# Kernel optimization log

Measured on AMD Instinct MI355X. Metric: run time of the kernel, lower is better.

Reference implementation:

```python
import jax, jax.numpy as jnp
import numpy as np

N, E, G = 20000, 320000, 64
F, ED, H, HID, DL, DOUT = 128, 32, 300, 600, 256, 128
BN_INV = np.float32(1.0 / np.sqrt(1.0 + 1e-5))  # eval-mode BatchNorm, running stats (0,1)
EPS = 1e-7


def setup_inputs() -> dict:
    key = jax.random.key(0)
    ks = jax.random.split(key, 24)
    rn = lambda k, shape, s=0.05: (jax.random.normal(k, shape, jnp.float32) * s)
    inp = {
        "x": rn(ks[0], (N, F), 1.0),
        "edge_attr": rn(ks[1], (E, ED), 1.0),
        "edge_index": jax.random.randint(ks[2], (2, E), 0, N),
        "batch": jnp.sort(jax.random.randint(ks[3], (N,), 0, G)),
        # GENConv params (lin_src/lin_edge/lin_dst have bias=False in PyG)
        "W_src": rn(ks[4], (F, H)),
        "W_edge": rn(ks[5], (ED, H)),
        "W_dst": rn(ks[6], (F, H)),
        # GENConv internal MLP: [H, 2H, 2H, H], Linear -> ReLU -> BatchNorm between
        "W1": rn(ks[7], (H, HID)), "b1": jnp.zeros((HID,), jnp.float32),
        "g1": jnp.ones((HID,), jnp.float32), "be1": jnp.zeros((HID,), jnp.float32),
        "W2": rn(ks[8], (HID, HID)), "b2": jnp.zeros((HID,), jnp.float32),
        "g2": jnp.ones((HID,), jnp.float32), "be2": jnp.zeros((HID,), jnp.float32),
        "W3": rn(ks[9], (HID, H)), "b3": jnp.zeros((H,), jnp.float32),
        # encoder head: Linear(H,256) -> ReLU -> Linear(256, d_out)
        "L1": rn(ks[10], (H, DL)), "bl1": jnp.zeros((DL,), jnp.float32),
        "L2": rn(ks[11], (DL, DOUT)), "bl2": jnp.zeros((DOUT,), jnp.float32),
    }
    return inp


def reference(x, edge_attr, W_src, W_edge, W_dst, W1, b1, g1, be1, W2, b2, g2, be2,
              W3, b3, L1, bl1, L2, bl2, edge_index, batch):
    src, dst = edge_index[0], edge_index[1]
    h = x @ W_src                                   # [N,H]
    e = edge_attr @ W_edge                          # [E,H]
    msg = jax.nn.relu(h[src] + e) + EPS             # [E,H]
    # softmax aggregation over incoming edges, per destination node, per channel (t=1)
    m = jax.ops.segment_max(msg, dst, num_segments=N)          # [N,H]
    ex = jnp.exp(msg - m[dst])                                 # [E,H]
    denom = jax.ops.segment_sum(ex, dst, num_segments=N)       # [N,H]
    alpha = ex / denom[dst]
    agg = jax.ops.segment_sum(msg * alpha, dst, num_segments=N)  # [N,H]
    out = agg + x @ W_dst                                        # residual with lin_dst(x)
    # GENConv MLP (act_first: Linear -> ReLU -> BN), eval-mode BN
    h1 = jax.nn.relu(out @ W1 + b1) * BN_INV * g1 + be1
    h2 = jax.nn.relu(h1 @ W2 + b2) * BN_INV * g2 + be2
    out = h2 @ W3 + b3                                           # [N,H]
    # encoder linear stack (dropout = identity in eval)
    out = jax.nn.relu(out @ L1 + bl1)
    out = out @ L2 + bl2                                         # [N, d_out]
    # global mean pool over graphs
    cnt = jax.ops.segment_sum(jnp.ones((N,), jnp.float32), batch, num_segments=G)
    pooled = jax.ops.segment_sum(out, batch, num_segments=G) / jnp.maximum(cnt, 1.0)[:, None]
    return pooled
```

## Files before the change

kernel.cpp:

```cpp
#include <hip/hip_runtime.h>
#include <stdint.h>
#include <stddef.h>

#define N_NODES  20000
#define N_EDGES  320000
#define N_GRAPH  64
#define F_IN     128
#define E_DIM    32
#define H_DIM    300
#define HID_DIM  600
#define DL_DIM   256
#define DOUT_DIM 128
#define BN_INV_F 0.9999950000374997f
#define EPS_MSG  1e-7f

typedef _Float16 f16;
typedef __attribute__((ext_vector_type(8))) _Float16 f16x8;
typedef __attribute__((ext_vector_type(4))) _Float16 f16x4;
typedef __attribute__((ext_vector_type(4))) float f32x4;

#define GLOAD_LDS16(gp, lp) \
    __builtin_amdgcn_global_load_lds( \
        (const __attribute__((address_space(1))) void*)(gp), \
        (__attribute__((address_space(3))) void*)(lp), 16, 0, 0)

template<bool HAS_BIAS, bool RELU, bool BN, int OUT_MODE, bool DUAL_A>
__global__ __launch_bounds__(256)
void hgemm(const f16* __restrict__ A, const f16* __restrict__ A2,
           const f16* __restrict__ Bt,
           const float* __restrict__ bias, const float* __restrict__ gamma,
           const float* __restrict__ beta,
           void* __restrict__ O1, void* __restrict__ O2,
           int M, int Nreal, int Kpad, int ostride, int npad)
{
    __shared__ __align__(16) f16 As[64][32];
    __shared__ __align__(16) f16 Bs[64][32];
    const int tid  = threadIdx.x;
    const int bm   = blockIdx.y * 64;
    const int bn   = blockIdx.x * 64;
    const int wave = tid >> 6;
    const int lane = tid & 63;
    const int wm   = (wave >> 1) * 32;
    const int wn   = (wave & 1) * 32;
    const int fr   = lane & 15;
    const int kg   = lane >> 4;
    const int srow = tid >> 2;
    const int cg   = tid & 3;
    const int gsw  = (cg - (srow >> 1)) & 3;

    const f32x4 z = {0.f, 0.f, 0.f, 0.f};
    f32x4 acc[2][2] = {{z, z}, {z, z}};

    const f16* Asrc  = A + (size_t)(bm + srow) * Kpad + gsw * 8;
    const f16* Bsrc  = Bt + (size_t)(bn + srow) * Kpad + gsw * 8;
    const f16* A2src = DUAL_A ? (A2 + (size_t)(bm + srow) * Kpad + gsw * 8) : nullptr;
    f16* AsDst = &As[0][0] + (size_t)tid * 8;
    f16* BsDst = &Bs[0][0] + (size_t)tid * 8;
    const bool avalid = (bm + srow) < M;
    const f16x8 zf = {(f16)0, (f16)0, (f16)0, (f16)0,
                      (f16)0, (f16)0, (f16)0, (f16)0};

    const int ra0 = wm + fr,      ra1 = wm + 16 + fr;
    const int rb0 = wn + fr,      rb1 = wn + 16 + fr;
    const f16* a0p = &As[ra0][(((ra0 >> 1) + kg) & 3) * 8];
    const f16* a1p = &As[ra1][(((ra1 >> 1) + kg) & 3) * 8];
    const f16* b0p = &Bs[rb0][(((rb0 >> 1) + kg) & 3) * 8];
    const f16* b1p = &Bs[rb1][(((rb1 >> 1) + kg) & 3) * 8];

    for (int k0 = 0; k0 < Kpad; k0 += 32) {
        if (DUAL_A) {
            f16x8 va = zf;
            if (avalid)
                va = *(const f16x8*)Asrc + *(const f16x8*)A2src;
            *(f16x8*)AsDst = va;
            GLOAD_LDS16(Bsrc, BsDst);
            if (DUAL_A) { Asrc += 32; A2src += 32; }
        } else {
            GLOAD_LDS16(Asrc, AsDst);
            GLOAD_LDS16(Bsrc, BsDst);
            Asrc += 32;
        }
        Bsrc += 32;
        __syncthreads();
        f16x8 a0 = *(const f16x8*)a0p;
        f16x8 a1 = *(const f16x8*)a1p;
        f16x8 b0 = *(const f16x8*)b0p;
        f16x8 b1 = *(const f16x8*)b1p;
        acc[0][0] = __builtin_amdgcn_mfma_f32_16x16x32_f16(a0, b0, acc[0][0], 0, 0, 0);
        acc[0][1] = __builtin_amdgcn_mfma_f32_16x16x32_f16(a0, b1, acc[0][1], 0, 0, 0);
        acc[1][0] = __builtin_amdgcn_mfma_f32_16x16x32_f16(a1, b0, acc[1][0], 0, 0, 0);
        acc[1][1] = __builtin_amdgcn_mfma_f32_16x16x32_f16(a1, b1, acc[1][1], 0, 0, 0);
        __syncthreads();
    }

    #pragma unroll
    for (int mi = 0; mi < 2; ++mi) {
        #pragma unroll
        for (int r = 0; r < 4; ++r) {
            int row = bm + wm + mi * 16 + kg * 4 + r;
            if (row >= M) continue;
            #pragma unroll
            for (int ni = 0; ni < 2; ++ni) {
                int col = bn + wn + ni * 16 + fr;
                float v = acc[mi][ni][r];
                if (OUT_MODE == 2) {
                    if (col < 300)
                        ((f16*)O1)[(size_t)row * 304 + col] = (f16)v;
                    else if (col < 600)
                        ((f16*)O2)[(size_t)row * 320 + (col - 300)] = (f16)v;
                    else if (col < 620)
                        ((f16*)O2)[(size_t)row * 320 + (col - 300)] = (f16)0.f;
                } else {
                    if (col < Nreal) {
                        if (HAS_BIAS) v += bias[col];
                        if (RELU)     v = fmaxf(v, 0.f);
                        if (BN)       v = v * (BN_INV_F * gamma[col]) + beta[col];
                        if (OUT_MODE == 0)
                            ((float*)O1)[(size_t)row * ostride + col] = v;
                        else
                            ((f16*)O1)[(size_t)row * ostride + col] = (f16)v;
                    } else if (OUT_MODE == 1 && col < npad) {
                        ((f16*)O1)[(size_t)row * ostride + col] = (f16)0.f;
                    }
                }
            }
        }
    }
}

#define XB_N   640000
#define WSD_N  76800
#define WT1_N  192000
#define WT2_N  364800
#define WT3_N  182400
#define WL1_N  81920
#define WL2_N  32768
#define WET_N  9728
#define ZC_N   20000
#define ZP_N   8256
#define CAST_TOTAL (XB_N+WSD_N+WT1_N+WT2_N+WT3_N+WL1_N+WL2_N+WET_N+ZC_N+ZP_N)

__global__ __launch_bounds__(256)
void cast_all(const float* __restrict__ x,
              const float* __restrict__ Wsrc, const float* __restrict__ Wdst,
              const float* __restrict__ W1, const float* __restrict__ W2,
              const float* __restrict__ W3, const float* __restrict__ L1,
              const float* __restrict__ L2, const float* __restrict__ We,
              f16* __restrict__ xb,
              f16* __restrict__ Wt_sd, f16* __restrict__ Wt1,
              f16* __restrict__ Wt2, f16* __restrict__ Wt3,
              f16* __restrict__ WtL1, f16* __restrict__ WtL2,
              f16* __restrict__ Wet,
              int* __restrict__ cnts, float* __restrict__ pool,
              float* __restrict__ cnt)
{
    int t = blockIdx.x * 256 + threadIdx.x;
    if (t < XB_N) {
        float4 v = ((const float4*)x)[t];
        f16x4 o = {(f16)v.x, (f16)v.y, (f16)v.z, (f16)v.w};
        ((f16x4*)xb)[t] = o;
        return;
    }
    t -= XB_N;
    if (t < WSD_N) {
        int n = t / 128, k = t % 128;
        const float* W = (n < 300) ? Wsrc : Wdst;
        int nn = (n < 300) ? n : n - 300;
        Wt_sd[t] = (f16)W[(size_t)k * 300 + nn];
        return;
    }
    t -= WSD_N;
    if (t < WT1_N) {
        int n = t / 320, k = t % 320;
        Wt1[t] = (f16)((k < 300) ? W1[(size_t)k * 600 + n] : 0.f);
        return;
    }
    t -= WT1_N;
    if (t < WT2_N) {
        int n = t / 608, k = t % 608;
        Wt2[t] = (f16)((k < 600) ? W2[(size_t)k * 600 + n] : 0.f);
        return;
    }
    t -= WT2_N;
    if (t < WT3_N) {
        int n = t / 608, k = t % 608;
        Wt3[t] = (f16)((k < 600) ? W3[(size_t)k * 300 + n] : 0.f);
        return;
    }
    t -= WT3_N;
    if (t < WL1_N) {
        int n = t / 320, k = t % 320;
        WtL1[t] = (f16)((k < 300) ? L1[(size_t)k * 256 + n] : 0.f);
        return;
    }
    t -= WL1_N;
    if (t < WL2_N) {
        int n = t / 256, k = t % 256;
        WtL2[t] = (f16)L2[(size_t)k * 128 + n];
        return;
    }
    t -= WL2_N;
    if (t < WET_N) {
        int n = t / 32, k = t % 32;
        Wet[t] = (f16)((n < 300) ? We[(size_t)k * 300 + n] : 0.f);
        return;
    }
    t -= WET_N;
    if (t < ZC_N) { cnts[t] = 0; return; }
    t -= ZC_N;
    if (t < ZP_N) {
        if (t < 8192) pool[t] = 0.f;
        else          cnt[t - 8192] = 0.f;
    }
}

__global__ __launch_bounds__(256)
void hist_kernel(const int* __restrict__ ei, int* __restrict__ counts)
{
    for (int e = blockIdx.x * 256 + threadIdx.x; e < N_EDGES; e += gridDim.x * 256)
        atomicAdd(&counts[ei[N_EDGES + e]], 1);
}

__global__ __launch_bounds__(256)
void scan1_kernel(const int* __restrict__ counts, int* __restrict__ rowptr,
                  int* __restrict__ bsum)
{
    __shared__ int sd[256];
    int tid = threadIdx.x;
    int i = blockIdx.x * 256 + tid;
    int v = (i < N_NODES) ? counts[i] : 0;
    sd[tid] = v;
    __syncthreads();
    #pragma unroll
    for (int off = 1; off < 256; off <<= 1) {
        int t = (tid >= off) ? sd[tid - off] : 0;
        __syncthreads();
        sd[tid] += t;
        __syncthreads();
    }
    if (i < N_NODES) rowptr[i + 1] = sd[tid];
    if (tid == 255) bsum[blockIdx.x] = sd[255];
}

__global__ __launch_bounds__(128)
void scan2_kernel(const int* __restrict__ bsum, int* __restrict__ boffs, int nb)
{
    __shared__ int sd[128];
    int tid = threadIdx.x;
    int v = (tid < nb) ? bsum[tid] : 0;
    sd[tid] = v;
    __syncthreads();
    #pragma unroll
    for (int off = 1; off < 128; off <<= 1) {
        int t = (tid >= off) ? sd[tid - off] : 0;
        __syncthreads();
        sd[tid] += t;
        __syncthreads();
    }
    if (tid < nb) boffs[tid] = sd[tid] - v;
}

__global__ __launch_bounds__(256)
void scan3_kernel(int* __restrict__ rowptr, int* __restrict__ shadow,
                  const int* __restrict__ boffs)
{
    int i = blockIdx.x * 256 + threadIdx.x;
    if (i < N_NODES) {
        int v = rowptr[i + 1] + boffs[blockIdx.x];
        rowptr[i + 1] = v;
        shadow[i + 1] = v;
    }
    if (i == 0) { rowptr[0] = 0; shadow[0] = 0; }
}

__global__ __launch_bounds__(256)
void scatter_gather(const float* __restrict__ ea, const int* __restrict__ ei,
                    int* __restrict__ shadow, f16* __restrict__ eaf,
                    int* __restrict__ srcs)
{
    int e = blockIdx.x * 256 + threadIdx.x;
    if (e >= N_EDGES) return;
    int d = ei[N_EDGES + e];
    int pos = atomicAdd(&shadow[d], 1);
    srcs[pos] = ei[e];
    const float4* src = (const float4*)(ea + (size_t)e * E_DIM);
    f16* dst = eaf + (size_t)pos * E_DIM;
    #pragma unroll
    for (int q = 0; q < 8; ++q) {
        float4 v = src[q];
        f16x4 o = {(f16)v.x, (f16)v.y, (f16)v.z, (f16)v.w};
        ((f16x4*)dst)[q] = o;
    }
}

#define NPB 10
#define CHK 32
#define ELDS_STRIDE 308

__global__ __launch_bounds__(320, 1)
void agg_mfma(const f16* __restrict__ hf, const f16* __restrict__ eaf,
              const int* __restrict__ srcs, const int* __restrict__ rptr,
              const f16* __restrict__ Wet, f16* __restrict__ aggb)
{
    __shared__ __align__(16) f16 As[CHK][40];
    __shared__ __align__(16) f16 e_lds[CHK * ELDS_STRIDE];
    __shared__ int s_lds[CHK];

    const int tid  = threadIdx.x;
    const int w    = tid >> 6;
    const int lane = tid & 63;
    const int fr   = lane & 15;
    const int kg   = lane >> 4;
    const int c    = tid;
    const bool act = c < H_DIM;
    const int cc   = c < 304 ? c : 303;

    const int n0 = blockIdx.x * NPB;
    const int n1 = n0 + NPB;
    const int P0 = rptr[n0];
    const int P1 = rptr[n1];

    f16x8 bf0, bf1, bf2, bf3;
    {
        int t0 = w;
        bf0 = *(const f16x8*)(Wet + (size_t)(t0 * 16 + fr) * 32 + kg * 8);
        bf1 = *(const f16x8*)(Wet + (size_t)((t0 + 5) * 16 + fr) * 32 + kg * 8);
        bf2 = *(const f16x8*)(Wet + (size_t)((t0 + 10) * 16 + fr) * 32 + kg * 8);
        if (t0 + 15 < 19)
            bf3 = *(const f16x8*)(Wet + (size_t)((t0 + 15) * 16 + fr) * 32 + kg * 8);
    }

    const f32x4 z4 = {0.f, 0.f, 0.f, 0.f};

    int n_cur = n0;
    int e_end = (n_cur < n1) ? rptr[n_cur + 1] : 0x7fffffff;
    float num = 0.f, den = 0.f;

    auto flush = [&]() {
        float agg = den > 0.f ? num / den : 0.f;
        aggb[(size_t)n_cur * 320 + c] = act ? (f16)agg : (f16)0.f;
        num = 0.f; den = 0.f;
        ++n_cur;
        e_end = (n_cur < n1) ? rptr[n_cur + 1] : 0x7fffffff;
    };

    for (int ck = P0; ck < P1; ck += CHK) {
        const int cend = min(ck + CHK, P1);
        if (tid < 128) {
            int row = tid >> 2;
            int kq  = (tid & 3) * 8;
            int p   = ck + row;
            if (p >= N_EDGES) p = N_EDGES - 1;
            *(f16x8*)&As[row][kq] = *(const f16x8*)(eaf + (size_t)p * E_DIM + kq);
        } else if (tid < 128 + CHK) {
            int j = tid - 128;
            int p = ck + j;
            s_lds[j] = srcs[p < N_EDGES ? p : N_EDGES - 1];
        }
        __syncthreads();
        {
            f16x8 af0 = *(const f16x8*)&As[fr][kg * 8];
            f16x8 af1 = *(const f16x8*)&As[16 + fr][kg * 8];
            #pragma unroll
            for (int i = 0; i < 4; ++i) {
                int t = w + 5 * i;
                if (t >= 19) continue;
                f16x8 bf = (i == 0) ? bf0 : (i == 1) ? bf1 : (i == 2) ? bf2 : bf3;
                #pragma unroll
                for (int mi = 0; mi < 2; ++mi) {
                    f16x8 af = (mi == 0) ? af0 : af1;
                    f32x4 d = __builtin_amdgcn_mfma_f32_16x16x32_f16(af, bf, z4, 0, 0, 0);
                    int col = t * 16 + fr;
                    int rbase = mi * 16 + kg * 4;
                    #pragma unroll
                    for (int r = 0; r < 4; ++r)
                        e_lds[(size_t)(rbase + r) * ELDS_STRIDE + col] = (f16)d[r];
                }
            }
        }
        __syncthreads();
        for (int ck2 = ck; ck2 < cend; ck2 += 16) {
            float hv[16], ev[16];
            #pragma unroll
            for (int j = 0; j < 16; ++j) {
                int idx = (ck2 - ck) + j;
                int s = s_lds[idx];
                hv[j] = (float)hf[(size_t)s * 304 + cc];
                ev[j] = (float)e_lds[(size_t)idx * ELDS_STRIDE + cc];
            }
            #pragma unroll
            for (int j = 0; j < 16; ++j) {
                int p = ck2 + j;
                if (p < cend) {
                    while (p == e_end) flush();
                    float msg = fmaxf(hv[j] + ev[j], 0.f) + EPS_MSG;
                    float ex = __expf(msg);
                    den += ex;
                    num += msg * ex;
                }
            }
        }
        __syncthreads();
    }
    while (n_cur < n1) flush();
}

#define POOL_NPB 128
__global__ __launch_bounds__(128)
void pool_seg(const float* __restrict__ out3, const int* __restrict__ batch,
              float* __restrict__ pooled, float* __restrict__ cnt)
{
    int c = threadIdx.x;
    int n0 = blockIdx.x * POOL_NPB;
    int n1 = min(n0 + POOL_NPB, N_NODES);
    int g = batch[n0];
    float s = 0.f, cn = 0.f;
    for (int n = n0; n < n1; ++n) {
        int gn = batch[n];
        if (gn != g) {
            atomicAdd(&pooled[(size_t)g * DOUT_DIM + c], s);
            if (c == 0) atomicAdd(&cnt[g], cn);
            g = gn; s = 0.f; cn = 0.f;
        }
        s += out3[(size_t)n * DOUT_DIM + c];
        cn += 1.f;
    }
    atomicAdd(&pooled[(size_t)g * DOUT_DIM + c], s);
    if (c == 0) atomicAdd(&cnt[g], cn);
}

__global__ __launch_bounds__(256)
void finalize_kernel(const float* __restrict__ pooled, const float* __restrict__ cnt,
                     float* __restrict__ out)
{
    int i = blockIdx.x * 256 + threadIdx.x;
    if (i >= N_GRAPH * DOUT_DIM) return;
    out[i] = pooled[i] / fmaxf(cnt[i / DOUT_DIM], 1.f);
}

extern "C" void kernel_launch(void* const* d_in, const int* in_sizes, int n_in,
                              void* d_out, int out_size, void* d_ws, size_t ws_size,
                              hipStream_t stream)
{
    const float* x      = (const float*)d_in[0];
    const float* ea     = (const float*)d_in[1];
    const int*   eidx   = (const int*)d_in[2];
    const int*   batch  = (const int*)d_in[3];
    const float* W_src  = (const float*)d_in[4];
    const float* W_edge = (const float*)d_in[5];
    const float* W_dst  = (const float*)d_in[6];
    const float* W1     = (const float*)d_in[7];
    const float* b1     = (const float*)d_in[8];
    const float* g1     = (const float*)d_in[9];
    const float* be1    = (const float*)d_in[10];
    const float* W2     = (const float*)d_in[11];
    const float* b2     = (const float*)d_in[12];
    const float* g2     = (const float*)d_in[13];
    const float* be2    = (const float*)d_in[14];
    const float* W3     = (const float*)d_in[15];
    const float* b3     = (const float*)d_in[16];
    const float* L1     = (const float*)d_in[17];
    const float* bl1    = (const float*)d_in[18];
    const float* L2     = (const float*)d_in[19];
    const float* bl2    = (const float*)d_in[20];
    float* out = (float*)d_out;
    char* ws = (char*)d_ws;

    f16*   ws_h     = (f16*)  (ws + 0);
    f16*   ws_b2b   = (f16*)  (ws + 0);
    float* ws_out3  = (float*)(ws + 0);
    f16*   ws_eaf   = (f16*)  (ws + 24320000);
    f16*   ws_b1b   = (f16*)  (ws + 24320000);
    f16*   ws_out1b = (f16*)  (ws + 24320000);
    f16*   ws_out2b = (f16*)  (ws + 37120000);
    f16*   ws_aggb  = (f16*)  (ws + 44800000);
    f16*   ws_out0b = (f16*)  (ws + 65280000);
    f16*   ws_xb    = (f16*)  (ws + 78080000);
    f16*   ws_wtsd  = (f16*)  (ws + 83200000);
    f16*   ws_wt1   = (f16*)  (ws + 83353600);
    f16*   ws_wt2   = (f16*)  (ws + 83737600);
    f16*   ws_wt3   = (f16*)  (ws + 84467200);
    f16*   ws_wtl1  = (f16*)  (ws + 84832000);
    f16*   ws_wtl2  = (f16*)  (ws + 84995840);
    f16*   ws_wet   = (f16*)  (ws + 85061376);
    int*   ws_cnts  = (int*)  (ws + 85080832);
    int*   ws_rptr  = (int*)  (ws + 85240832);
    int*   ws_shad  = (int*)  (ws + 85320848);
    int*   ws_srcs  = (int*)  (ws + 86600848);
    float* ws_pool  = (float*)(ws + 87880848);
    float* ws_cnt   = (float*)(ws + 87913616);
    int*   ws_bsum  = (int*)  (ws + 87913872);
    int*   ws_boffs = (int*)  (ws + 87914384);

    dim3 blk(256);

    cast_all<<<(CAST_TOTAL + 255) / 256, blk, 0, stream>>>(
        x, W_src, W_dst, W1, W2, W3, L1, L2, W_edge,
        ws_xb, ws_wtsd, ws_wt1, ws_wt2, ws_wt3, ws_wtl1, ws_wtl2, ws_wet,
        ws_cnts, ws_pool, ws_cnt);

    hgemm<false, false, false, 2, false><<<dim3(10, 313), blk, 0, stream>>>(
        ws_xb, nullptr, ws_wtsd, nullptr, nullptr, nullptr, ws_h, ws_out0b,
        N_NODES, 600, 128, 304, 608);

    hist_kernel<<<512, blk, 0, stream>>>(eidx, ws_cnts);
    {
        int nb = (N_NODES + 255) / 256;
        scan1_kernel<<<nb, blk, 0, stream>>>(ws_cnts, ws_rptr, ws_bsum);
        scan2_kernel<<<1, dim3(128), 0, stream>>>(ws_bsum, ws_boffs, nb);
        scan3_kernel<<<nb, blk, 0, stream>>>(ws_rptr, ws_shad, ws_boffs);
    }
    scatter_gather<<<(N_EDGES + 255) / 256, blk, 0, stream>>>(
        ea, eidx, ws_shad, ws_eaf, ws_srcs);

    agg_mfma<<<N_NODES / NPB, dim3(320), 0, stream>>>(
        ws_h, ws_eaf, ws_srcs, ws_rptr, ws_wet, ws_aggb);

    hgemm<true, true, true, 1, true><<<dim3(10, 313), blk, 0, stream>>>(
        ws_aggb, ws_out0b, ws_wt1, b1, g1, be1, ws_b1b, nullptr,
        N_NODES, 600, 320, 608, 608);
    hgemm<true, true, true, 1, false><<<dim3(10, 313), blk, 0, stream>>>(
        ws_b1b, nullptr, ws_wt2, b2, g2, be2, ws_b2b, nullptr,
        N_NODES, 600, 608, 608, 608);
    hgemm<true, false, false, 1, false><<<dim3(5, 313), blk, 0, stream>>>(
        ws_b2b, nullptr, ws_wt3, b3, nullptr, nullptr, ws_out1b, nullptr,
        N_NODES, 300, 608, 320, 320);
    hgemm<true, true, false, 1, false><<<dim3(4, 313), blk, 0, stream>>>(
        ws_out1b, nullptr, ws_wtl1, bl1, nullptr, nullptr, ws_out2b, nullptr,
        N_NODES, 256, 320, 256, 256);
    hgemm<true, false, false, 0, false><<<dim3(2, 313), blk, 0, stream>>>(
        ws_out2b, nullptr, ws_wtl2, bl2, nullptr, nullptr, ws_out3, nullptr,
        N_NODES, 128, 256, 128, 128);

    pool_seg<<<(N_NODES + POOL_NPB - 1) / POOL_NPB, dim3(128), 0, stream>>>(
        ws_out3, batch, ws_pool, ws_cnt);
    finalize_kernel<<<(N_GRAPH * DOUT_DIM + 255) / 256, blk, 0, stream>>>(
        ws_pool, ws_cnt, out);
}
```

Before: 338.6 us.

## Fuse residual into aggregation, fuse pooling into last GEMM, merge scan passes

The aggregation kernel now adds its softmax result directly into the lin_dst residual buffer, so the first MLP GEMM loads a single A operand through global_load_lds instead of summing two buffers in registers. The final linear GEMM scatters its outputs with atomicAdd into per-graph pool sums, which removes the fp32 out3 buffer and the pool_seg kernel. Graph counts are recomputed in finalize by binary search on the sorted batch array. The three-pass scan becomes two passes, with each block serially summing the preceding block sums. The trade-off is heavy atomic contention on the 64x128 pool array (20000 rows onto 64 graphs).

```diff
diff --git a/kernel.cpp b/kernel.cpp
--- a/kernel.cpp
+++ b/kernel.cpp
@@ -24,13 +24,13 @@
         (const __attribute__((address_space(1))) void*)(gp), \
         (__attribute__((address_space(3))) void*)(lp), 16, 0, 0)
 
-template<bool HAS_BIAS, bool RELU, bool BN, int OUT_MODE, bool DUAL_A>
-__global__ __launch_bounds__(256)
-void hgemm(const f16* __restrict__ A, const f16* __restrict__ A2,
-           const f16* __restrict__ Bt,
+template<bool HAS_BIAS, bool RELU, bool BN, int OUT_MODE>
+__global__ __launch_bounds__(256)
+void hgemm(const f16* __restrict__ A, const f16* __restrict__ Bt,
            const float* __restrict__ bias, const float* __restrict__ gamma,
            const float* __restrict__ beta,
            void* __restrict__ O1, void* __restrict__ O2,
+           const int* __restrict__ batchp,
            int M, int Nreal, int Kpad, int ostride, int npad)
 {
     __shared__ __align__(16) f16 As[64][32];
@@ -51,14 +51,10 @@
     const f32x4 z = {0.f, 0.f, 0.f, 0.f};
     f32x4 acc[2][2] = {{z, z}, {z, z}};
 
-    const f16* Asrc  = A + (size_t)(bm + srow) * Kpad + gsw * 8;
-    const f16* Bsrc  = Bt + (size_t)(bn + srow) * Kpad + gsw * 8;
-    const f16* A2src = DUAL_A ? (A2 + (size_t)(bm + srow) * Kpad + gsw * 8) : nullptr;
+    const f16* Asrc = A + (size_t)(bm + srow) * Kpad + gsw * 8;
+    const f16* Bsrc = Bt + (size_t)(bn + srow) * Kpad + gsw * 8;
     f16* AsDst = &As[0][0] + (size_t)tid * 8;
     f16* BsDst = &Bs[0][0] + (size_t)tid * 8;
-    const bool avalid = (bm + srow) < M;
-    const f16x8 zf = {(f16)0, (f16)0, (f16)0, (f16)0,
-                      (f16)0, (f16)0, (f16)0, (f16)0};
 
     const int ra0 = wm + fr,      ra1 = wm + 16 + fr;
     const int rb0 = wn + fr,      rb1 = wn + 16 + fr;
@@ -68,18 +64,9 @@
     const f16* b1p = &Bs[rb1][(((rb1 >> 1) + kg) & 3) * 8];
 
     for (int k0 = 0; k0 < Kpad; k0 += 32) {
-        if (DUAL_A) {
-            f16x8 va = zf;
-            if (avalid)
-                va = *(const f16x8*)Asrc + *(const f16x8*)A2src;
-            *(f16x8*)AsDst = va;
-            GLOAD_LDS16(Bsrc, BsDst);
-            if (DUAL_A) { Asrc += 32; A2src += 32; }
-        } else {
-            GLOAD_LDS16(Asrc, AsDst);
-            GLOAD_LDS16(Bsrc, BsDst);
-            Asrc += 32;
-        }
+        GLOAD_LDS16(Asrc, AsDst);
+        GLOAD_LDS16(Bsrc, BsDst);
+        Asrc += 32;
         Bsrc += 32;
         __syncthreads();
         f16x8 a0 = *(const f16x8*)a0p;
@@ -110,6 +97,11 @@
                         ((f16*)O2)[(size_t)row * 320 + (col - 300)] = (f16)v;
                     else if (col < 620)
                         ((f16*)O2)[(size_t)row * 320 + (col - 300)] = (f16)0.f;
+                } else if (OUT_MODE == 3) {
+                    if (col < Nreal) {
+                        if (HAS_BIAS) v += bias[col];
+                        atomicAdd(&((float*)O2)[(size_t)batchp[row] * DOUT_DIM + col], v);
+                    }
                 } else {
                     if (col < Nreal) {
                         if (HAS_BIAS) v += bias[col];
@@ -137,7 +129,7 @@
 #define WL2_N  32768
 #define WET_N  9728
 #define ZC_N   20000
-#define ZP_N   8256
+#define ZP_N   8192
 #define CAST_TOTAL (XB_N+WSD_N+WT1_N+WT2_N+WT3_N+WL1_N+WL2_N+WET_N+ZC_N+ZP_N)
 
 __global__ __launch_bounds__(256)
@@ -151,8 +143,7 @@
               f16* __restrict__ Wt2, f16* __restrict__ Wt3,
               f16* __restrict__ WtL1, f16* __restrict__ WtL2,
               f16* __restrict__ Wet,
-              int* __restrict__ cnts, float* __restrict__ pool,
-              float* __restrict__ cnt)
+              int* __restrict__ cnts, float* __restrict__ pooled)
 {
     int t = blockIdx.x * 256 + threadIdx.x;
     if (t < XB_N) {
@@ -208,10 +199,7 @@
     t -= WET_N;
     if (t < ZC_N) { cnts[t] = 0; return; }
     t -= ZC_N;
-    if (t < ZP_N) {
-        if (t < 8192) pool[t] = 0.f;
-        else          cnt[t - 8192] = 0.f;
-    }
+    if (t < ZP_N) pooled[t] = 0.f;
 }
 
 __global__ __launch_bounds__(256)
@@ -222,8 +210,8 @@
 }
 
 __global__ __launch_bounds__(256)
-void scan1_kernel(const int* __restrict__ counts, int* __restrict__ rowptr,
-                  int* __restrict__ bsum)
+void scan_a(const int* __restrict__ counts, int* __restrict__ rowptr,
+            int* __restrict__ bsum)
 {
     __shared__ int sd[256];
     int tid = threadIdx.x;
@@ -242,31 +230,21 @@
     if (tid == 255) bsum[blockIdx.x] = sd[255];
 }
 
-__global__ __launch_bounds__(128)
-void scan2_kernel(const int* __restrict__ bsum, int* __restrict__ boffs, int nb)
-{
-    __shared__ int sd[128];
+__global__ __launch_bounds__(256)
+void scan_b(int* __restrict__ rowptr, int* __restrict__ shadow,
+            const int* __restrict__ bsum)
+{
+    __shared__ int off_s;
     int tid = threadIdx.x;
-    int v = (tid < nb) ? bsum[tid] : 0;
-    sd[tid] = v;
+    if (tid == 0) {
+        int o = 0;
+        for (int b = 0; b < (int)blockIdx.x; ++b) o += bsum[b];
+        off_s = o;
+    }
     __syncthreads();
-    #pragma unroll
-    for (int off = 1; off < 128; off <<= 1) {
-        int t = (tid >= off) ? sd[tid - off] : 0;
-        __syncthreads();
-        sd[tid] += t;
-        __syncthreads();
-    }
-    if (tid < nb) boffs[tid] = sd[tid] - v;
-}
-
-__global__ __launch_bounds__(256)
-void scan3_kernel(int* __restrict__ rowptr, int* __restrict__ shadow,
-                  const int* __restrict__ boffs)
-{
-    int i = blockIdx.x * 256 + threadIdx.x;
+    int i = blockIdx.x * 256 + tid;
     if (i < N_NODES) {
-        int v = rowptr[i + 1] + boffs[blockIdx.x];
+        int v = rowptr[i + 1] + off_s;
         rowptr[i + 1] = v;
         shadow[i + 1] = v;
     }
@@ -300,7 +278,7 @@
 __global__ __launch_bounds__(320, 1)
 void agg_mfma(const f16* __restrict__ hf, const f16* __restrict__ eaf,
               const int* __restrict__ srcs, const int* __restrict__ rptr,
-              const f16* __restrict__ Wet, f16* __restrict__ aggb)
+              const f16* __restrict__ Wet, f16* __restrict__ out0b)
 {
     __shared__ __align__(16) f16 As[CHK][40];
     __shared__ __align__(16) f16 e_lds[CHK * ELDS_STRIDE];
@@ -338,7 +316,10 @@
 
     auto flush = [&]() {
         float agg = den > 0.f ? num / den : 0.f;
-        aggb[(size_t)n_cur * 320 + c] = act ? (f16)agg : (f16)0.f;
+        if (act) {
+            size_t idx = (size_t)n_cur * 320 + c;
+            out0b[idx] = (f16)(agg + (float)out0b[idx]);
+        }
         num = 0.f; den = 0.f;
         ++n_cur;
         e_end = (n_cur < n1) ? rptr[n_cur + 1] : 0x7fffffff;
@@ -405,37 +386,25 @@
     while (n_cur < n1) flush();
 }
 
-#define POOL_NPB 128
-__global__ __launch_bounds__(128)
-void pool_seg(const float* __restrict__ out3, const int* __restrict__ batch,
-              float* __restrict__ pooled, float* __restrict__ cnt)
-{
-    int c = threadIdx.x;
-    int n0 = blockIdx.x * POOL_NPB;
-    int n1 = min(n0 + POOL_NPB, N_NODES);
-    int g = batch[n0];
-    float s = 0.f, cn = 0.f;
-    for (int n = n0; n < n1; ++n) {
-        int gn = batch[n];
-        if (gn != g) {
-            atomicAdd(&pooled[(size_t)g * DOUT_DIM + c], s);
-            if (c == 0) atomicAdd(&cnt[g], cn);
-            g = gn; s = 0.f; cn = 0.f;
-        }
-        s += out3[(size_t)n * DOUT_DIM + c];
-        cn += 1.f;
-    }
-    atomicAdd(&pooled[(size_t)g * DOUT_DIM + c], s);
-    if (c == 0) atomicAdd(&cnt[g], cn);
-}
-
-__global__ __launch_bounds__(256)
-void finalize_kernel(const float* __restrict__ pooled, const float* __restrict__ cnt,
+__device__ __forceinline__ int lower_bound_batch(const int* b, int key)
+{
+    int lo = 0, hi = N_NODES;
+    while (lo < hi) {
+        int mid = (lo + hi) >> 1;
+        if (b[mid] < key) lo = mid + 1; else hi = mid;
+    }
+    return lo;
+}
+
+__global__ __launch_bounds__(256)
+void finalize_kernel(const float* __restrict__ pooled, const int* __restrict__ batch,
                      float* __restrict__ out)
 {
     int i = blockIdx.x * 256 + threadIdx.x;
     if (i >= N_GRAPH * DOUT_DIM) return;
-    out[i] = pooled[i] / fmaxf(cnt[i / DOUT_DIM], 1.f);
+    int g = i / DOUT_DIM;
+    int cnt = lower_bound_batch(batch, g + 1) - lower_bound_batch(batch, g);
+    out[i] = pooled[i] / fmaxf((float)cnt, 1.f);
 }
 
 extern "C" void kernel_launch(void* const* d_in, const int* in_sizes, int n_in,
@@ -467,73 +436,66 @@
     char* ws = (char*)d_ws;
 
     f16*   ws_h     = (f16*)  (ws + 0);
+    f16*   ws_xb    = (f16*)  (ws + 12160000);
+    f16*   ws_eaf   = (f16*)  (ws + 17280000);
+    int*   ws_srcs  = (int*)  (ws + 37760000);
+    f16*   ws_out0b = (f16*)  (ws + 39040000);
+    f16*   ws_b1b   = (f16*)  (ws + 51840000);
     f16*   ws_b2b   = (f16*)  (ws + 0);
-    float* ws_out3  = (float*)(ws + 0);
-    f16*   ws_eaf   = (f16*)  (ws + 24320000);
-    f16*   ws_b1b   = (f16*)  (ws + 24320000);
     f16*   ws_out1b = (f16*)  (ws + 24320000);
     f16*   ws_out2b = (f16*)  (ws + 37120000);
-    f16*   ws_aggb  = (f16*)  (ws + 44800000);
-    f16*   ws_out0b = (f16*)  (ws + 65280000);
-    f16*   ws_xb    = (f16*)  (ws + 78080000);
-    f16*   ws_wtsd  = (f16*)  (ws + 83200000);
-    f16*   ws_wt1   = (f16*)  (ws + 83353600);
-    f16*   ws_wt2   = (f16*)  (ws + 83737600);
-    f16*   ws_wt3   = (f16*)  (ws + 84467200);
-    f16*   ws_wtl1  = (f16*)  (ws + 84832000);
-    f16*   ws_wtl2  = (f16*)  (ws + 84995840);
-    f16*   ws_wet   = (f16*)  (ws + 85061376);
-    int*   ws_cnts  = (int*)  (ws + 85080832);
-    int*   ws_rptr  = (int*)  (ws + 85240832);
-    int*   ws_shad  = (int*)  (ws + 85320848);
-    int*   ws_srcs  = (int*)  (ws + 86600848);
-    float* ws_pool  = (float*)(ws + 87880848);
-    float* ws_cnt   = (float*)(ws + 87913616);
-    int*   ws_bsum  = (int*)  (ws + 87913872);
-    int*   ws_boffs = (int*)  (ws + 87914384);
+    f16*   ws_wtsd  = (f16*)  (ws + 76160000);
+    f16*   ws_wt1   = (f16*)  (ws + 76313600);
+    f16*   ws_wt2   = (f16*)  (ws + 76697600);
+    f16*   ws_wt3   = (f16*)  (ws + 77427200);
+    f16*   ws_wtl1  = (f16*)  (ws + 77792000);
+    f16*   ws_wtl2  = (f16*)  (ws + 77955840);
+    f16*   ws_wet   = (f16*)  (ws + 78021376);
+    int*   ws_cnts  = (int*)  (ws + 78040832);
+    int*   ws_rptr  = (int*)  (ws + 78120832);
+    int*   ws_shad  = (int*)  (ws + 78200848);
+    int*   ws_bsum  = (int*)  (ws + 78280864);
+    float* ws_pool  = (float*)(ws + 78281248);
 
     dim3 blk(256);
 
     cast_all<<<(CAST_TOTAL + 255) / 256, blk, 0, stream>>>(
         x, W_src, W_dst, W1, W2, W3, L1, L2, W_edge,
         ws_xb, ws_wtsd, ws_wt1, ws_wt2, ws_wt3, ws_wtl1, ws_wtl2, ws_wet,
-        ws_cnts, ws_pool, ws_cnt);
-
-    hgemm<false, false, false, 2, false><<<dim3(10, 313), blk, 0, stream>>>(
-        ws_xb, nullptr, ws_wtsd, nullptr, nullptr, nullptr, ws_h, ws_out0b,
+        ws_cnts, ws_pool);
+
+    hgemm<false, false, false, 2><<<dim3(10, 313), blk, 0, stream>>>(
+        ws_xb, ws_wtsd, nullptr, nullptr, nullptr, ws_h, ws_out0b, nullptr,
         N_NODES, 600, 128, 304, 608);
 
     hist_kernel<<<512, blk, 0, stream>>>(eidx, ws_cnts);
     {
         int nb = (N_NODES + 255) / 256;
-        scan1_kernel<<<nb, blk, 0, stream>>>(ws_cnts, ws_rptr, ws_bsum);
-        scan2_kernel<<<1, dim3(128), 0, stream>>>(ws_bsum, ws_boffs, nb);
-        scan3_kernel<<<nb, blk, 0, stream>>>(ws_rptr, ws_shad, ws_boffs);
+        scan_a<<<nb, blk, 0, stream>>>(ws_cnts, ws_rptr, ws_bsum);
+        scan_b<<<nb, blk, 0, stream>>>(ws_rptr, ws_shad, ws_bsum);
     }
     scatter_gather<<<(N_EDGES + 255) / 256, blk, 0, stream>>>(
         ea, eidx, ws_shad, ws_eaf, ws_srcs);
 
     agg_mfma<<<N_NODES / NPB, dim3(320), 0, stream>>>(
-        ws_h, ws_eaf, ws_srcs, ws_rptr, ws_wet, ws_aggb);
-
-    hgemm<true, true, true, 1, true><<<dim3(10, 313), blk, 0, stream>>>(
-        ws_aggb, ws_out0b, ws_wt1, b1, g1, be1, ws_b1b, nullptr,
+        ws_h, ws_eaf, ws_srcs, ws_rptr, ws_wet, ws_out0b);
+
+    hgemm<true, true, true, 1><<<dim3(10, 313), blk, 0, stream>>>(
+        ws_out0b, ws_wt1, b1, g1, be1, ws_b1b, nullptr, nullptr,
         N_NODES, 600, 320, 608, 608);
-    hgemm<true, true, true, 1, false><<<dim3(10, 313), blk, 0, stream>>>(
-        ws_b1b, nullptr, ws_wt2, b2, g2, be2, ws_b2b, nullptr,
+    hgemm<true, true, true, 1><<<dim3(10, 313), blk, 0, stream>>>(
+        ws_b1b, ws_wt2, b2, g2, be2, ws_b2b, nullptr, nullptr,
         N_NODES, 600, 608, 608, 608);
-    hgemm<true, false, false, 1, false><<<dim3(5, 313), blk, 0, stream>>>(
-        ws_b2b, nullptr, ws_wt3, b3, nullptr, nullptr, ws_out1b, nullptr,
+    hgemm<true, false, false, 1><<<dim3(5, 313), blk, 0, stream>>>(
+        ws_b2b, ws_wt3, b3, nullptr, nullptr, ws_out1b, nullptr, nullptr,
         N_NODES, 300, 608, 320, 320);
-    hgemm<true, true, false, 1, false><<<dim3(4, 313), blk, 0, stream>>>(
-        ws_out1b, nullptr, ws_wtl1, bl1, nullptr, nullptr, ws_out2b, nullptr,
+    hgemm<true, true, false, 1><<<dim3(4, 313), blk, 0, stream>>>(
+        ws_out1b, ws_wtl1, bl1, nullptr, nullptr, ws_out2b, nullptr, nullptr,
         N_NODES, 256, 320, 256, 256);
-    hgemm<true, false, false, 0, false><<<dim3(2, 313), blk, 0, stream>>>(
-        ws_out2b, nullptr, ws_wtl2, bl2, nullptr, nullptr, ws_out3, nullptr,
+    hgemm<true, false, false, 3><<<dim3(2, 313), blk, 0, stream>>>(
+        ws_out2b, ws_wtl2, bl2, nullptr, nullptr, nullptr, ws_pool, batch,
         N_NODES, 128, 256, 128, 128);
 
-    pool_seg<<<(N_NODES + POOL_NPB - 1) / POOL_NPB, dim3(128), 0, stream>>>(
-        ws_out3, batch, ws_pool, ws_cnt);
     finalize_kernel<<<(N_GRAPH * DOUT_DIM + 255) / 256, blk, 0, stream>>>(
-        ws_pool, ws_cnt, out);
-}
+        ws_pool, batch, out);
+}
```

Measured after the change: 330.0 us. 1.03x faster.
